# Optimization experiments

Measured on AMD Instinct MI355X. Metric: run time of the kernel, lower is better.

The kernel has to match this reference:

```python
import jax, jax.numpy as jnp
import numpy as np

B, S, D = 8, 1024, 1152
H, HD = 16, 72  # num_heads, head_dim

def setup_inputs() -> dict:
    key = jax.random.key(0)
    ks = jax.random.split(key, 7)
    hidden_states = jax.random.normal(ks[0], (B, S, D), dtype=jnp.float32)
    cos = jax.random.uniform(ks[1], (S, HD), dtype=jnp.float32)
    sin = jax.random.uniform(ks[2], (S, HD), dtype=jnp.float32)
    qkv_w = jax.random.normal(ks[3], (3 * D, D), dtype=jnp.float32) * 0.02
    qkv_b = jnp.zeros((3 * D,), dtype=jnp.float32)
    proj_w = jax.random.normal(ks[4], (D, D), dtype=jnp.float32) * 0.02
    proj_b = jnp.zeros((D,), dtype=jnp.float32)
    return {"hidden_states": hidden_states, "cos": cos, "sin": sin,
            "qkv_w": qkv_w, "qkv_b": qkv_b, "proj_w": proj_w, "proj_b": proj_b}

def _rotate_half(x):
    x1, x2 = jnp.split(x, 2, axis=-1)
    return jnp.concatenate((-x2, x1), axis=-1)

def reference(hidden_states, cos, sin, qkv_w, qkv_b, proj_w, proj_b):
    b, s, d = hidden_states.shape
    # fused QKV projection
    qkv = hidden_states @ qkv_w.T + qkv_b            # [B,S,3D]
    qkv = qkv.reshape(b, s, 3, H, HD)
    qkv = jnp.transpose(qkv, (2, 0, 3, 1, 4))        # [3,B,H,S,HD]
    q, k, v = qkv[0], qkv[1], qkv[2]
    # rotary embedding, cos/sin broadcast [1,1,S,HD]
    c = cos[None, None, :, :]
    sn = sin[None, None, :, :]
    q = q * c + _rotate_half(q) * sn
    k = k * c + _rotate_half(k) * sn
    # SDPA
    scale = HD ** -0.5
    scores = jnp.einsum('bhqd,bhkd->bhqk', q, k) * scale
    probs = jax.nn.softmax(scores, axis=-1)
    attn = jnp.einsum('bhqk,bhkd->bhqd', probs, v)   # [B,H,S,HD]
    attn = jnp.transpose(attn, (0, 2, 1, 3)).reshape(b, s, d)
    return attn @ proj_w.T + proj_b
```

## Files before the change

### kernel.cpp

```cpp
#include <hip/hip_runtime.h>
#include <hip/hip_bf16.h>


typedef __attribute__((ext_vector_type(8))) short short8;
typedef __attribute__((ext_vector_type(4))) float f32x4;

__device__ __forceinline__ float bflo(unsigned int u) { return __uint_as_float(u << 16); }

__device__ __forceinline__ unsigned int f2bf(float f) {
    unsigned int u = __float_as_uint(f);
    return (u + 0x7FFFu + ((u >> 16) & 1u)) >> 16;
}

__device__ __forceinline__ void stout(float* C, size_t idx, float v) { C[idx] = v; }
__device__ __forceinline__ void stout(__hip_bfloat16* C, size_t idx, float v) {
    C[idx] = __float2bfloat16(v);
}

__device__ __forceinline__ void async_cp16(const void* g, void* l) {
    __builtin_amdgcn_global_load_lds((const __attribute__((address_space(1))) void*)g,
                                     (__attribute__((address_space(3))) void*)l, 16, 0, 0);
}

__global__ void f32_to_bf16_pair(
    const float* __restrict__ s0, unsigned short* __restrict__ d0, int n0_4,
    const float* __restrict__ s1, unsigned short* __restrict__ d1, int n1_4)
{
    int i = blockIdx.x * 256 + threadIdx.x;
    const float* s; unsigned short* d;
    if (i < n0_4) { s = s0; d = d0; }
    else if (i < n0_4 + n1_4) { s = s1; d = d1; i -= n0_4; }
    else return;
    float4 f = ((const float4*)s)[i];
    ushort4 r;
    r.x = (unsigned short)f2bf(f.x);
    r.y = (unsigned short)f2bf(f.y);
    r.z = (unsigned short)f2bf(f.z);
    r.w = (unsigned short)f2bf(f.w);
    ((ushort4*)d)[i] = r;
}

template <typename OT>
__global__ __launch_bounds__(256, 2) void gemm_bt_lds(
    const __hip_bfloat16* __restrict__ A,
    const __hip_bfloat16* __restrict__ B,
    const float* __restrict__ bias,
    OT* __restrict__ C,
    int M, int N, int K)
{
    __shared__ __align__(16) unsigned short As[128 * 32];
    __shared__ __align__(16) unsigned short Bs[128 * 32];

    const int tid  = threadIdx.x;
    const int lane = tid & 63;
    const int w    = tid >> 6;
    const int wr   = w >> 1;
    const int wc   = w & 1;
    const int bm   = blockIdx.y * 128;
    const int bn   = blockIdx.x * 128;

    const int lrow = lane >> 2;
    const int lcol = (lane & 3) * 8;

    const unsigned short* ag[2];
    const unsigned short* bg[2];
    unsigned short* al[2];
    unsigned short* bl[2];
#pragma unroll
    for (int c = 0; c < 2; c++) {
        const int r = w * 32 + c * 16 + lrow;
        ag[c] = (const unsigned short*)A + (size_t)(bm + r) * K + lcol;
        bg[c] = (const unsigned short*)B + (size_t)(bn + r) * K + lcol;
        al[c] = &As[(w * 2 + c) * 512];
        bl[c] = &Bs[(w * 2 + c) * 512];
    }

    f32x4 acc[4][4];
#pragma unroll
    for (int i = 0; i < 4; i++)
#pragma unroll
        for (int j = 0; j < 4; j++)
            acc[i][j] = (f32x4){0.f, 0.f, 0.f, 0.f};

    const int kq = (lane >> 4) * 8;
    const int fr = lane & 15;

    for (int k0 = 0; k0 < K; k0 += 32) {
        __syncthreads();
#pragma unroll
        for (int c = 0; c < 2; c++) {
            async_cp16(ag[c] + k0, al[c]);
            async_cp16(bg[c] + k0, bl[c]);
        }
        __syncthreads();

        short8 af[4], bf[4];
#pragma unroll
        for (int i = 0; i < 4; i++)
            af[i] = *(const short8*)&As[(wr * 64 + i * 16 + fr) * 32 + kq];
#pragma unroll
        for (int j = 0; j < 4; j++)
            bf[j] = *(const short8*)&Bs[(wc * 64 + j * 16 + fr) * 32 + kq];
#pragma unroll
        for (int i = 0; i < 4; i++)
#pragma unroll
            for (int j = 0; j < 4; j++)
                acc[i][j] = __builtin_amdgcn_mfma_f32_16x16x32_bf16(af[i], bf[j], acc[i][j], 0, 0, 0);
    }

#pragma unroll
    for (int i = 0; i < 4; i++) {
        const int mrow = bm + wr * 64 + i * 16 + (lane >> 4) * 4;
#pragma unroll
        for (int j = 0; j < 4; j++) {
            const int ncol = bn + wc * 64 + j * 16 + fr;
            const float bv = bias[ncol];
#pragma unroll
            for (int r = 0; r < 4; r++) {
                stout(C, (size_t)(mrow + r) * N + ncol, acc[i][j][r] + bv);
            }
        }
    }
}

__global__ void rope_qk(
    const __hip_bfloat16* __restrict__ qkv,
    const float* __restrict__ cosp,
    const float* __restrict__ sinp,
    __hip_bfloat16* __restrict__ Qo,
    __hip_bfloat16* __restrict__ Ko)
{
    const int tid = blockIdx.x * 256 + threadIdx.x;
    const int total = 8 * 16 * 1024 * 36;
    if (tid >= total) return;
    const int i    = tid % 36;
    const int rest = tid / 36;
    const int s    = rest & 1023;
    const int bh   = rest >> 10;

    const size_t row = (size_t)((bh >> 4) * 1024 + s) * 3456;
    const int col = (bh & 15) * 72 + i;

    const float c1 = cosp[s * 72 + i];
    const float c2 = cosp[s * 72 + i + 36];
    const float s1 = sinp[s * 72 + i];
    const float s2 = sinp[s * 72 + i + 36];

    const float qa = __bfloat162float(qkv[row + col]);
    const float qb = __bfloat162float(qkv[row + col + 36]);
    const float ka = __bfloat162float(qkv[row + 1152 + col]);
    const float kb = __bfloat162float(qkv[row + 1152 + col + 36]);

    const size_t ob = ((size_t)bh * 1024 + s) * 72 + i;
    const float QS = 0.17002324f;

    Qo[ob]      = __float2bfloat16((qa * c1 - qb * s1) * QS);
    Qo[ob + 36] = __float2bfloat16((qb * c2 + qa * s2) * QS);
    Ko[ob]      = __float2bfloat16(ka * c1 - kb * s1);
    Ko[ob + 36] = __float2bfloat16(kb * c2 + ka * s2);
}

__global__ void v_transpose(
    const __hip_bfloat16* __restrict__ qkv,
    __hip_bfloat16* __restrict__ Vt)
{
    __shared__ __align__(16) unsigned short T[64 * 72];
    const int tid = threadIdx.x;
    const int bh = blockIdx.x >> 4;
    const int st = blockIdx.x & 15;
    const unsigned short* src = (const unsigned short*)qkv
        + ((size_t)(bh >> 4) * 1024 + st * 64) * 3456 + 2304 + (bh & 15) * 72;

#pragma unroll
    for (int k = 0; k < 3; k++) {
        const int c = tid + k * 256;
        if (c < 576) {
            const int s = c / 9, off = (c % 9) * 8;
            *(uint4*)&T[c * 8] = *(const uint4*)(src + (size_t)s * 3456 + off);
        }
    }
    __syncthreads();

    unsigned short* dst = (unsigned short*)Vt + (size_t)(bh * 16 + st) * 72 * 64;
#pragma unroll
    for (int k = 0; k < 9; k++) {
        const int o = tid + k * 256;
        const int d = o >> 5;
        const int sl = (o & 31) * 2;
        ushort2 v;
        v.x = T[sl * 72 + d];
        v.y = T[(sl + 1) * 72 + d];
        *(ushort2*)&dst[d * 64 + sl] = v;
    }
}

__global__ __launch_bounds__(256, 4) void attn_mfma(
    const __hip_bfloat16* __restrict__ Q,
    const __hip_bfloat16* __restrict__ K,
    const __hip_bfloat16* __restrict__ Vt,
    __hip_bfloat16* __restrict__ O)
{
    __shared__ __align__(16) unsigned short Ks[64][88];
    __shared__ __align__(16) unsigned short Vs[80][88];
    __shared__ __align__(16) unsigned short Ps[4][16][88];

    const int tid  = threadIdx.x;
    const int lane = tid & 63;
    const int w    = tid >> 6;
    const int quad = lane >> 4;
    const int fr   = lane & 15;
    const int bh   = blockIdx.x & 127;
    const int qt   = blockIdx.x >> 7;
    const int qbase = qt * 64 + w * 16;

    const short8 z8 = (short8){0,0,0,0,0,0,0,0};

    for (int idx = tid; idx < 8 * 88; idx += 256)
        Vs[72 + idx / 88][idx % 88] = (idx < 88) ? (unsigned short)0x3F80 : (unsigned short)0;

    const unsigned short* qp = (const unsigned short*)Q + ((size_t)bh * 1024 + qbase + fr) * 72;
    short8 qf[3];
    qf[0] = *(const short8*)(qp + quad * 8);
    qf[1] = *(const short8*)(qp + 32 + quad * 8);
    qf[2] = (quad == 0) ? *(const short8*)(qp + 64) : z8;

    f32x4 Oa[5];
#pragma unroll
    for (int n = 0; n < 5; n++) Oa[n] = (f32x4){0.f, 0.f, 0.f, 0.f};

    const unsigned short* kg0 = (const unsigned short*)K + (size_t)bh * 1024 * 72;
    const unsigned short* vg0 = (const unsigned short*)Vt + (size_t)bh * 16 * 72 * 64;

#pragma unroll 1
    for (int t = 0; t < 16; t++) {
        __syncthreads();
        const unsigned short* kg = kg0 + (size_t)t * 64 * 72;
        const unsigned short* vg = vg0 + (size_t)t * 72 * 64;
#pragma unroll
        for (int k = 0; k < 3; k++) {
            const int c = tid + k * 256;
            if (c < 576) {
                const int row = c / 9, off = (c % 9) * 8;
                *(uint4*)&Ks[row][off] = *(const uint4*)(kg + c * 8);
                *(uint4*)&Vs[c >> 3][(c & 7) * 8] = *(const uint4*)(vg + c * 8);
            }
        }
        __syncthreads();

        f32x4 sc[4];
#pragma unroll
        for (int nt = 0; nt < 4; nt++) {
            short8 b0 = *(const short8*)&Ks[nt * 16 + fr][quad * 8];
            short8 b1 = *(const short8*)&Ks[nt * 16 + fr][32 + quad * 8];
            short8 b2 = (quad == 0) ? *(const short8*)&Ks[nt * 16 + fr][64] : z8;
            f32x4 s = (f32x4){0.f, 0.f, 0.f, 0.f};
            s = __builtin_amdgcn_mfma_f32_16x16x32_bf16(qf[0], b0, s, 0, 0, 0);
            s = __builtin_amdgcn_mfma_f32_16x16x32_bf16(qf[1], b1, s, 0, 0, 0);
            s = __builtin_amdgcn_mfma_f32_16x16x32_bf16(qf[2], b2, s, 0, 0, 0);
            sc[nt] = s;
        }

#pragma unroll
        for (int nt = 0; nt < 4; nt++)
#pragma unroll
            for (int r = 0; r < 4; r++)
                Ps[w][quad * 4 + r][nt * 16 + fr] =
                    (unsigned short)f2bf(exp2f(sc[nt][r]));

#pragma unroll
        for (int ks = 0; ks < 2; ks++) {
            short8 ap = *(const short8*)&Ps[w][fr][ks * 32 + quad * 8];
#pragma unroll
            for (int n = 0; n < 5; n++) {
                short8 bv = *(const short8*)&Vs[n * 16 + fr][ks * 32 + quad * 8];
                Oa[n] = __builtin_amdgcn_mfma_f32_16x16x32_bf16(ap, bv, Oa[n], 0, 0, 0);
            }
        }
    }

    const int lsrc = (lane & 48) | 8;
    float inv[4];
#pragma unroll
    for (int r = 0; r < 4; r++)
        inv[r] = 1.f / __shfl(Oa[4][r], lsrc, 64);

    const int b = bh >> 4, h = bh & 15;
    unsigned short* ob = (unsigned short*)O;
#pragma unroll
    for (int n = 0; n < 5; n++) {
        const int d = n * 16 + fr;
        if (d < 72) {
#pragma unroll
            for (int r = 0; r < 4; r++) {
                const size_t idx = ((size_t)b * 1024 + qbase + quad * 4 + r) * 1152 + h * 72 + d;
                ob[idx] = (unsigned short)f2bf(Oa[n][r] * inv[r]);
            }
        }
    }
}

extern "C" void kernel_launch(void* const* d_in, const int* in_sizes, int n_in,
                              void* d_out, int out_size, void* d_ws, size_t ws_size,
                              hipStream_t stream)
{
    const float* hs     = (const float*)d_in[0];
    const float* cosp   = (const float*)d_in[1];
    const float* sinp   = (const float*)d_in[2];
    const float* qkv_w  = (const float*)d_in[3];
    const float* qkv_b  = (const float*)d_in[4];
    const float* proj_w = (const float*)d_in[5];
    const float* proj_b = (const float*)d_in[6];
    float* out = (float*)d_out;

    char* ws = (char*)d_ws;
    __hip_bfloat16* qkv_buf = (__hip_bfloat16*)ws;
    __hip_bfloat16* Qb = (__hip_bfloat16*)(ws + 56623104);
    __hip_bfloat16* Kb = Qb + 9437184;
    __hip_bfloat16* Vt = Kb + 9437184;
    __hip_bfloat16* Ab = qkv_buf;

    unsigned short* hs_bf = (unsigned short*)Qb;
    unsigned short* qw_bf = (unsigned short*)Kb;
    unsigned short* pw_bf = (unsigned short*)Qb;

    f32_to_bf16_pair<<<13104, 256, 0, stream>>>(hs, hs_bf, 2359296,
                                                qkv_w, qw_bf, 995328);
    gemm_bt_lds<__hip_bfloat16>
        <<<dim3(27, 64), 256, 0, stream>>>((const __hip_bfloat16*)hs_bf,
                                           (const __hip_bfloat16*)qw_bf,
                                           qkv_b, qkv_buf, 8192, 3456, 1152);
    rope_qk<<<18432, 256, 0, stream>>>(qkv_buf, cosp, sinp, Qb, Kb);
    v_transpose<<<2048, 256, 0, stream>>>(qkv_buf, Vt);
    attn_mfma<<<2048, 256, 0, stream>>>(Qb, Kb, Vt, Ab);
    f32_to_bf16_pair<<<1296, 256, 0, stream>>>(proj_w, pw_bf, 331776,
                                               nullptr, nullptr, 0);
    gemm_bt_lds<float>
        <<<dim3(9, 64), 256, 0, stream>>>((const __hip_bfloat16*)Ab,
                                          (const __hip_bfloat16*)pw_bf,
                                          proj_b, out, 8192, 1152, 1152);
}
```

Measured before the change: 350.6 us.

## Process two query sub-tiles per wave in attention to reuse K/V tiles

Each wave now handles 32 query rows instead of 16, so every K and V tile staged in LDS feeds twice as many MFMAs, and the grid shrinks to 1024 blocks. LDS row padding goes from 88 to 72 elements, which lets the K tile be copied contiguously and cuts LDS use. The cost is more registers per thread (two sets of Q fragments and accumulators), fewer blocks in flight, and possible LDS bank conflicts now that rows are unpadded.

```diff
diff --git a/kernel.cpp b/kernel.cpp
--- a/kernel.cpp
+++ b/kernel.cpp
@@ -200,9 +200,9 @@
     const __hip_bfloat16* __restrict__ Vt,
     __hip_bfloat16* __restrict__ O)
 {
-    __shared__ __align__(16) unsigned short Ks[64][88];
-    __shared__ __align__(16) unsigned short Vs[80][88];
-    __shared__ __align__(16) unsigned short Ps[4][16][88];
+    __shared__ __align__(16) unsigned short Ks[64][72];
+    __shared__ __align__(16) unsigned short Vs[80][72];
+    __shared__ __align__(16) unsigned short Ps[4][32][72];
 
     const int tid  = threadIdx.x;
     const int lane = tid & 63;
@@ -211,22 +211,28 @@
     const int fr   = lane & 15;
     const int bh   = blockIdx.x & 127;
     const int qt   = blockIdx.x >> 7;
-    const int qbase = qt * 64 + w * 16;
+    const int qbase = qt * 128 + w * 32;
 
     const short8 z8 = (short8){0,0,0,0,0,0,0,0};
 
-    for (int idx = tid; idx < 8 * 88; idx += 256)
-        Vs[72 + idx / 88][idx % 88] = (idx < 88) ? (unsigned short)0x3F80 : (unsigned short)0;
+    for (int idx = tid; idx < 8 * 72; idx += 256)
+        Vs[72 + idx / 72][idx % 72] = (idx < 72) ? (unsigned short)0x3F80 : (unsigned short)0;
 
     const unsigned short* qp = (const unsigned short*)Q + ((size_t)bh * 1024 + qbase + fr) * 72;
-    short8 qf[3];
-    qf[0] = *(const short8*)(qp + quad * 8);
-    qf[1] = *(const short8*)(qp + 32 + quad * 8);
-    qf[2] = (quad == 0) ? *(const short8*)(qp + 64) : z8;
-
-    f32x4 Oa[5];
-#pragma unroll
-    for (int n = 0; n < 5; n++) Oa[n] = (f32x4){0.f, 0.f, 0.f, 0.f};
+    short8 qf[2][3];
+#pragma unroll
+    for (int sub = 0; sub < 2; sub++) {
+        const unsigned short* qs = qp + sub * 16 * 72;
+        qf[sub][0] = *(const short8*)(qs + quad * 8);
+        qf[sub][1] = *(const short8*)(qs + 32 + quad * 8);
+        qf[sub][2] = (quad == 0) ? *(const short8*)(qs + 64) : z8;
+    }
+
+    f32x4 Oa[2][5];
+#pragma unroll
+    for (int sub = 0; sub < 2; sub++)
+#pragma unroll
+        for (int n = 0; n < 5; n++) Oa[sub][n] = (f32x4){0.f, 0.f, 0.f, 0.f};
 
     const unsigned short* kg0 = (const unsigned short*)K + (size_t)bh * 1024 * 72;
     const unsigned short* vg0 = (const unsigned short*)Vt + (size_t)bh * 16 * 72 * 64;
@@ -240,60 +246,64 @@
         for (int k = 0; k < 3; k++) {
             const int c = tid + k * 256;
             if (c < 576) {
-                const int row = c / 9, off = (c % 9) * 8;
-                *(uint4*)&Ks[row][off] = *(const uint4*)(kg + c * 8);
+                *(uint4*)&((unsigned short*)Ks)[c * 8] = *(const uint4*)(kg + c * 8);
                 *(uint4*)&Vs[c >> 3][(c & 7) * 8] = *(const uint4*)(vg + c * 8);
             }
         }
         __syncthreads();
 
-        f32x4 sc[4];
 #pragma unroll
         for (int nt = 0; nt < 4; nt++) {
             short8 b0 = *(const short8*)&Ks[nt * 16 + fr][quad * 8];
             short8 b1 = *(const short8*)&Ks[nt * 16 + fr][32 + quad * 8];
             short8 b2 = (quad == 0) ? *(const short8*)&Ks[nt * 16 + fr][64] : z8;
-            f32x4 s = (f32x4){0.f, 0.f, 0.f, 0.f};
-            s = __builtin_amdgcn_mfma_f32_16x16x32_bf16(qf[0], b0, s, 0, 0, 0);
-            s = __builtin_amdgcn_mfma_f32_16x16x32_bf16(qf[1], b1, s, 0, 0, 0);
-            s = __builtin_amdgcn_mfma_f32_16x16x32_bf16(qf[2], b2, s, 0, 0, 0);
-            sc[nt] = s;
-        }
-
-#pragma unroll
-        for (int nt = 0; nt < 4; nt++)
-#pragma unroll
-            for (int r = 0; r < 4; r++)
-                Ps[w][quad * 4 + r][nt * 16 + fr] =
-                    (unsigned short)f2bf(exp2f(sc[nt][r]));
+            f32x4 s0 = (f32x4){0.f, 0.f, 0.f, 0.f};
+            f32x4 s1 = (f32x4){0.f, 0.f, 0.f, 0.f};
+            s0 = __builtin_amdgcn_mfma_f32_16x16x32_bf16(qf[0][0], b0, s0, 0, 0, 0);
+            s1 = __builtin_amdgcn_mfma_f32_16x16x32_bf16(qf[1][0], b0, s1, 0, 0, 0);
+            s0 = __builtin_amdgcn_mfma_f32_16x16x32_bf16(qf[0][1], b1, s0, 0, 0, 0);
+            s1 = __builtin_amdgcn_mfma_f32_16x16x32_bf16(qf[1][1], b1, s1, 0, 0, 0);
+            s0 = __builtin_amdgcn_mfma_f32_16x16x32_bf16(qf[0][2], b2, s0, 0, 0, 0);
+            s1 = __builtin_amdgcn_mfma_f32_16x16x32_bf16(qf[1][2], b2, s1, 0, 0, 0);
+#pragma unroll
+            for (int r = 0; r < 4; r++) {
+                Ps[w][quad * 4 + r][nt * 16 + fr]      = (unsigned short)f2bf(exp2f(s0[r]));
+                Ps[w][16 + quad * 4 + r][nt * 16 + fr] = (unsigned short)f2bf(exp2f(s1[r]));
+            }
+        }
 
 #pragma unroll
         for (int ks = 0; ks < 2; ks++) {
-            short8 ap = *(const short8*)&Ps[w][fr][ks * 32 + quad * 8];
+            short8 ap0 = *(const short8*)&Ps[w][fr][ks * 32 + quad * 8];
+            short8 ap1 = *(const short8*)&Ps[w][16 + fr][ks * 32 + quad * 8];
 #pragma unroll
             for (int n = 0; n < 5; n++) {
                 short8 bv = *(const short8*)&Vs[n * 16 + fr][ks * 32 + quad * 8];
-                Oa[n] = __builtin_amdgcn_mfma_f32_16x16x32_bf16(ap, bv, Oa[n], 0, 0, 0);
+                Oa[0][n] = __builtin_amdgcn_mfma_f32_16x16x32_bf16(ap0, bv, Oa[0][n], 0, 0, 0);
+                Oa[1][n] = __builtin_amdgcn_mfma_f32_16x16x32_bf16(ap1, bv, Oa[1][n], 0, 0, 0);
             }
         }
     }
 
     const int lsrc = (lane & 48) | 8;
-    float inv[4];
-#pragma unroll
-    for (int r = 0; r < 4; r++)
-        inv[r] = 1.f / __shfl(Oa[4][r], lsrc, 64);
-
     const int b = bh >> 4, h = bh & 15;
     unsigned short* ob = (unsigned short*)O;
 #pragma unroll
-    for (int n = 0; n < 5; n++) {
-        const int d = n * 16 + fr;
-        if (d < 72) {
-#pragma unroll
-            for (int r = 0; r < 4; r++) {
-                const size_t idx = ((size_t)b * 1024 + qbase + quad * 4 + r) * 1152 + h * 72 + d;
-                ob[idx] = (unsigned short)f2bf(Oa[n][r] * inv[r]);
+    for (int sub = 0; sub < 2; sub++) {
+        float inv[4];
+#pragma unroll
+        for (int r = 0; r < 4; r++)
+            inv[r] = 1.f / __shfl(Oa[sub][4][r], lsrc, 64);
+#pragma unroll
+        for (int n = 0; n < 5; n++) {
+            const int d = n * 16 + fr;
+            if (d < 72) {
+#pragma unroll
+                for (int r = 0; r < 4; r++) {
+                    const size_t idx =
+                        ((size_t)b * 1024 + qbase + sub * 16 + quad * 4 + r) * 1152 + h * 72 + d;
+                    ob[idx] = (unsigned short)f2bf(Oa[sub][n][r] * inv[r]);
+                }
             }
         }
     }
@@ -331,7 +341,7 @@
                                            qkv_b, qkv_buf, 8192, 3456, 1152);
     rope_qk<<<18432, 256, 0, stream>>>(qkv_buf, cosp, sinp, Qb, Kb);
     v_transpose<<<2048, 256, 0, stream>>>(qkv_buf, Vt);
-    attn_mfma<<<2048, 256, 0, stream>>>(Qb, Kb, Vt, Ab);
+    attn_mfma<<<1024, 256, 0, stream>>>(Qb, Kb, Vt, Ab);
     f32_to_bf16_pair<<<1296, 256, 0, stream>>>(proj_w, pw_bf, 331776,
                                                nullptr, nullptr, 0);
     gemm_bt_lds<float>
```

Result: faster. 337.3 us (-3.8%).
